# Optimization experiments

Measured on AMD Instinct MI355X. Metric: run time of the kernel, lower is better.

## Reference

```python
import jax, jax.numpy as jnp
import numpy as np

NUM_HEADS = 16
D_MODEL = 1024
D_K = 64
D_V = 64
NEG_INF = -1e9


def setup_inputs() -> dict:
    key = jax.random.key(0)
    ks = jax.random.split(key, 7)
    B, S = 2, 2048
    Q = jax.random.normal(ks[0], (B, S, D_MODEL), dtype=jnp.float32)
    K = jax.random.normal(ks[1], (B, S, D_MODEL), dtype=jnp.float32)
    V = jax.random.normal(ks[2], (B, S, D_MODEL), dtype=jnp.float32)
    s = 1.0 / np.sqrt(D_MODEL)
    W_q = jax.random.normal(ks[3], (D_MODEL, D_K * NUM_HEADS), dtype=jnp.float32) * s
    W_k = jax.random.normal(ks[4], (D_MODEL, D_K), dtype=jnp.float32) * s
    W_v = jax.random.normal(ks[5], (D_MODEL, D_V), dtype=jnp.float32) * s
    W_o = jax.random.normal(ks[6], (D_V * NUM_HEADS, D_MODEL), dtype=jnp.float32) * (1.0 / np.sqrt(D_V * NUM_HEADS))
    return {"Q": Q, "K": K, "V": V, "W_q": W_q, "W_k": W_k, "W_v": W_v, "W_o": W_o}


def reference(Q, K, V, W_q, W_k, W_v, W_o):
    B, Sq, _ = Q.shape
    Sk = K.shape[1]
    # projections: Q -> per-head, K/V -> single shared head (MQA)
    q = (Q @ W_q).reshape(B, Sq, NUM_HEADS, D_K).transpose(0, 2, 1, 3)  # [B,H,Sq,Dk]
    k = K @ W_k  # [B,Sk,Dk]
    v = V @ W_v  # [B,Sk,Dv]
    scores = jnp.einsum('bhqd,bkd->bhqk', q, k) / jnp.sqrt(jnp.float32(D_K))
    causal = jnp.tril(jnp.ones((Sq, Sk), dtype=bool))  # [Sq,Sk]
    scores = jnp.where(causal[None, None], scores, NEG_INF)
    attn = jax.nn.softmax(scores, axis=-1)  # [B,H,Sq,Sk]
    out = jnp.einsum('bhqk,bkd->bhqd', attn, v)  # [B,H,Sq,Dv]
    out = out.transpose(0, 2, 1, 3).reshape(B, Sq, NUM_HEADS * D_V)
    return out @ W_o
```

## Files before the change

kernel.cpp:

```cpp
#include <hip/hip_runtime.h>
#include <hip/hip_bf16.h>
#include <cstdint>

typedef __bf16 bf16_t;
typedef __bf16 bf16x8 __attribute__((ext_vector_type(8)));
typedef __bf16 bf16x4 __attribute__((ext_vector_type(4)));
typedef float  floatx4 __attribute__((ext_vector_type(4)));

__device__ __forceinline__ bf16_t f2bf(float x) { return (bf16_t)x; }

__device__ __forceinline__ void gll16(const void* g, void* l) {
  __builtin_amdgcn_global_load_lds((const __attribute__((address_space(1))) void*)g,
                                   (__attribute__((address_space(3))) void*)l, 16, 0, 0);
}

#define S_LEN 2048
#define NHEAD 16
#define NTILE 32

__global__ __launch_bounds__(256) void cvt_bf16(const float* __restrict__ in,
                                                bf16_t* __restrict__ out, int n) {
  int idx = (blockIdx.x * 256 + threadIdx.x) * 4;
  int stride = gridDim.x * 256 * 4;
  for (; idx < n; idx += stride) {
    float4 v = *(const float4*)(in + idx);
    bf16x4 o;
    o[0] = f2bf(v.x); o[1] = f2bf(v.y); o[2] = f2bf(v.z); o[3] = f2bf(v.w);
    *(bf16x4*)(out + idx) = o;
  }
}

__global__ __launch_bounds__(256) void transpose_w2(const float* __restrict__ W0,
                                                    const float* __restrict__ W1,
                                                    bf16_t* __restrict__ O0,
                                                    bf16_t* __restrict__ O1,
                                                    int K, int N) {
  const float* W = blockIdx.z ? W1 : W0;
  bf16_t* Wt = blockIdx.z ? O1 : O0;
  __shared__ float tile[32][33];
  int n0 = blockIdx.x * 32, k0 = blockIdx.y * 32;
  int tx = threadIdx.x & 31, ty = threadIdx.x >> 5;
#pragma unroll
  for (int r = 0; r < 4; ++r)
    tile[ty + 8 * r][tx] = W[(size_t)(k0 + ty + 8 * r) * N + n0 + tx];
  __syncthreads();
#pragma unroll
  for (int r = 0; r < 4; ++r)
    Wt[(size_t)(n0 + ty + 8 * r) * K + k0 + tx] = f2bf(tile[tx][ty + 8 * r]);
}

template <int OUTMODE>
__global__ __launch_bounds__(256, 2) void gemm_async(const bf16_t* __restrict__ A,
                                                     const bf16_t* __restrict__ Bt,
                                                     void* __restrict__ Cout,
                                                     int M, int N, int K) {
  constexpr int BK = 32;
  __shared__ __align__(16) bf16_t As[64 * BK];
  __shared__ __align__(16) bf16_t Bs[128 * BK];
  const int tid = threadIdx.x;
  const int wave = tid >> 6, lane = tid & 63;
  const int quad = lane >> 4, lm = lane & 15;
  const int wr = wave >> 1, wc = wave & 1;
  const int m0 = blockIdx.x * 64, n0 = blockIdx.y * 128;

  floatx4 acc[2][4];
#pragma unroll
  for (int i = 0; i < 2; ++i)
#pragma unroll
    for (int j = 0; j < 4; ++j) acc[i][j] = (floatx4){0.f, 0.f, 0.f, 0.f};

  for (int k0 = 0; k0 < K; k0 += BK) {
    {
      int row = tid >> 2, c8 = tid & 3;
      gll16(A + (size_t)(m0 + row) * K + k0 + c8 * 8, As + wave * 512);
    }
#pragma unroll
    for (int rd = 0; rd < 2; ++rd) {
      int idx = rd * 256 + tid, row = idx >> 2, c8 = idx & 3;
      gll16(Bt + (size_t)(n0 + row) * K + k0 + c8 * 8, Bs + rd * 2048 + wave * 512);
    }
    __syncthreads();
    bf16x8 af[2], bfr[4];
#pragma unroll
    for (int i = 0; i < 2; ++i)
      af[i] = *(const bf16x8*)&As[(wr * 32 + i * 16 + lm) * BK + quad * 8];
#pragma unroll
    for (int j = 0; j < 4; ++j)
      bfr[j] = *(const bf16x8*)&Bs[(wc * 64 + j * 16 + lm) * BK + quad * 8];
#pragma unroll
    for (int i = 0; i < 2; ++i)
#pragma unroll
      for (int j = 0; j < 4; ++j)
        acc[i][j] = __builtin_amdgcn_mfma_f32_16x16x32_bf16(af[i], bfr[j],
                                                            acc[i][j], 0, 0, 0);
    __syncthreads();
  }
#pragma unroll
  for (int i = 0; i < 2; ++i) {
#pragma unroll
    for (int j = 0; j < 4; ++j) {
      int row0 = m0 + wr * 32 + i * 16 + quad * 4;
      int col = n0 + wc * 64 + j * 16 + lm;
#pragma unroll
      for (int r = 0; r < 4; ++r) {
        if constexpr (OUTMODE == 3)
          ((bf16_t*)Cout)[(size_t)(row0 + r) * N + col] = f2bf(acc[i][j][r] * 0.125f);
        else
          ((float*)Cout)[(size_t)(row0 + r) * N + col] = acc[i][j][r];
      }
    }
  }
}

__global__ __launch_bounds__(256) void gemm_kv(const float* __restrict__ Kin,
                                               const float* __restrict__ Vin,
                                               const bf16_t* __restrict__ Wkt,
                                               const bf16_t* __restrict__ Wvt,
                                               bf16_t* __restrict__ kp,
                                               bf16_t* __restrict__ vpt,
                                               int M, int K) {
  constexpr int BK = 32, LDK = 40, N = 64;
  const int isV = blockIdx.z;
  const float* A32 = isV ? Vin : Kin;
  const bf16_t* Bt = isV ? Wvt : Wkt;
  __shared__ __align__(16) bf16_t As[64 * LDK];
  __shared__ __align__(16) bf16_t Bs[64 * LDK];
  const int tid = threadIdx.x;
  const int wave = tid >> 6, lane = tid & 63;
  const int quad = lane >> 4, lm = lane & 15;
  const int wr = wave >> 1, wc = wave & 1;
  const int m0 = blockIdx.x * 64;

  floatx4 acc[2][2];
#pragma unroll
  for (int i = 0; i < 2; ++i)
#pragma unroll
    for (int j = 0; j < 2; ++j) acc[i][j] = (floatx4){0.f, 0.f, 0.f, 0.f};

  for (int k0 = 0; k0 < K; k0 += BK) {
    {
      int row = tid >> 2, c8 = tid & 3;
      const float* src = A32 + (size_t)(m0 + row) * K + k0 + c8 * 8;
      float4 f0 = *(const float4*)src;
      float4 f1 = *(const float4*)(src + 4);
      bf16x8 o;
      o[0] = f2bf(f0.x); o[1] = f2bf(f0.y); o[2] = f2bf(f0.z); o[3] = f2bf(f0.w);
      o[4] = f2bf(f1.x); o[5] = f2bf(f1.y); o[6] = f2bf(f1.z); o[7] = f2bf(f1.w);
      *(bf16x8*)&As[row * LDK + c8 * 8] = o;
    }
    {
      int row = tid >> 2, c8 = tid & 3;
      *(bf16x8*)&Bs[row * LDK + c8 * 8] =
          *(const bf16x8*)(Bt + (size_t)row * K + k0 + c8 * 8);
    }
    __syncthreads();
    bf16x8 af[2], bfr[2];
#pragma unroll
    for (int i = 0; i < 2; ++i)
      af[i] = *(const bf16x8*)&As[(wr * 32 + i * 16 + lm) * LDK + quad * 8];
#pragma unroll
    for (int j = 0; j < 2; ++j)
      bfr[j] = *(const bf16x8*)&Bs[(wc * 32 + j * 16 + lm) * LDK + quad * 8];
#pragma unroll
    for (int i = 0; i < 2; ++i)
#pragma unroll
      for (int j = 0; j < 2; ++j)
        acc[i][j] = __builtin_amdgcn_mfma_f32_16x16x32_bf16(af[i], bfr[j],
                                                            acc[i][j], 0, 0, 0);
    __syncthreads();
  }
#pragma unroll
  for (int i = 0; i < 2; ++i) {
#pragma unroll
    for (int j = 0; j < 2; ++j) {
      int row0 = m0 + wr * 32 + i * 16 + quad * 4;
      int col = wc * 32 + j * 16 + lm;
      if (isV) {
        bf16x4 o;
#pragma unroll
        for (int r = 0; r < 4; ++r) o[r] = f2bf(acc[i][j][r]);
        *(bf16x4*)&vpt[(size_t)col * M + row0] = o;
      } else {
#pragma unroll
        for (int r = 0; r < 4; ++r)
          kp[(size_t)(row0 + r) * N + col] = f2bf(acc[i][j][r]);
      }
    }
  }
}

__global__ __launch_bounds__(256, 2) void flash_mqa(const bf16_t* __restrict__ q,
                                                    const bf16_t* __restrict__ kk,
                                                    const bf16_t* __restrict__ vt,
                                                    bf16_t* __restrict__ O,
                                                    int BStot) {
  const int ta = blockIdx.x;
  const int tb = NTILE - 1 - ta;
  const int h = blockIdx.y, b = blockIdx.z;
  const int tid = threadIdx.x;
  const int wave = tid >> 6, lane = tid & 63;
  const int quad = lane >> 4, lm = lane & 15;

  __shared__ __align__(16) bf16_t k_lds[2][64 * 72];
  __shared__ __align__(16) bf16_t vt_lds[2][64 * 72];
  __shared__ __align__(16) bf16_t p_lds[4][16 * 72];

  const size_t bS = (size_t)b * S_LEN;
  const int qa = ta * 64, qb = tb * 64;

  bf16x8 qaf[2][2];
  {
    const bf16_t* qpA = q + (bS + qa + wave * 16 + lm) * 1024 + h * 64;
    const bf16_t* qpB = q + (bS + qb + wave * 16 + lm) * 1024 + h * 64;
    qaf[0][0] = *(const bf16x8*)(qpA + quad * 8);
    qaf[0][1] = *(const bf16x8*)(qpA + 32 + quad * 8);
    qaf[1][0] = *(const bf16x8*)(qpB + quad * 8);
    qaf[1][1] = *(const bf16x8*)(qpB + 32 + quad * 8);
  }

  bf16x8 onesf;
#pragma unroll
  for (int j = 0; j < 8; ++j) onesf[j] = f2bf(1.0f);

  floatx4 acc[2][4];
  floatx4 ps[2];
#pragma unroll
  for (int c = 0; c < 2; ++c) {
    ps[c] = (floatx4){0.f, 0.f, 0.f, 0.f};
#pragma unroll
    for (int t = 0; t < 4; ++t) acc[c][t] = (floatx4){0.f, 0.f, 0.f, 0.f};
  }

  const int srow = tid >> 3, sc8 = tid & 7;
  bf16x8 kst[2], vst[2];
  auto load_kv = [&](int kt) {
    const int k0 = kt * 64;
#pragma unroll
    for (int it = 0; it < 2; ++it) {
      int r = it * 32 + srow;
      kst[it] = *(const bf16x8*)(kk + (bS + k0 + r) * 64 + sc8 * 8);
      vst[it] = *(const bf16x8*)(vt + (size_t)r * BStot + bS + k0 + sc8 * 8);
    }
  };
  auto write_kv = [&](int buf) {
#pragma unroll
    for (int it = 0; it < 2; ++it) {
      int r = it * 32 + srow;
      *(bf16x8*)&k_lds[buf][r * 72 + sc8 * 8] = kst[it];
      *(bf16x8*)&vt_lds[buf][r * 72 + sc8 * 8] = vst[it];
    }
  };

  load_kv(0);
  write_kv(0);
  __syncthreads();

  for (int kt = 0; kt <= tb; ++kt) {
    const int cur = kt & 1;
    const int k0 = kt * 64;
    if (kt < tb) load_kv(kt + 1);

#pragma unroll
    for (int c = 0; c < 2; ++c) {
      const int myt = c ? tb : ta;
      if (kt > myt) continue;
      const int qrow0 = myt * 64 + wave * 16 + quad * 4;

      floatx4 s[4];
#pragma unroll
      for (int t = 0; t < 4; ++t) {
        const bf16_t* kb = &k_lds[cur][(t * 16 + lm) * 72 + quad * 8];
        bf16x8 b0 = *(const bf16x8*)kb;
        bf16x8 b1 = *(const bf16x8*)(kb + 32);
        floatx4 cc = (floatx4){0.f, 0.f, 0.f, 0.f};
        cc = __builtin_amdgcn_mfma_f32_16x16x32_bf16(qaf[c][0], b0, cc, 0, 0, 0);
        cc = __builtin_amdgcn_mfma_f32_16x16x32_bf16(qaf[c][1], b1, cc, 0, 0, 0);
        s[t] = cc;
      }
      if (kt == myt) {
#pragma unroll
        for (int t = 0; t < 4; ++t) {
          int kj = k0 + t * 16 + lm;
#pragma unroll
          for (int r = 0; r < 4; ++r)
            s[t][r] = (kj <= qrow0 + r) ? __expf(s[t][r]) : 0.f;
        }
      } else {
#pragma unroll
        for (int t = 0; t < 4; ++t)
#pragma unroll
          for (int r = 0; r < 4; ++r) s[t][r] = __expf(s[t][r]);
      }
#pragma unroll
      for (int t = 0; t < 4; ++t)
#pragma unroll
        for (int r = 0; r < 4; ++r)
          p_lds[wave][(quad * 4 + r) * 72 + t * 16 + lm] = f2bf(s[t][r]);

      bf16x8 a0 = *(const bf16x8*)&p_lds[wave][lm * 72 + quad * 8];
      bf16x8 a1 = *(const bf16x8*)&p_lds[wave][lm * 72 + 32 + quad * 8];
      ps[c] = __builtin_amdgcn_mfma_f32_16x16x32_bf16(a0, onesf, ps[c], 0, 0, 0);
      ps[c] = __builtin_amdgcn_mfma_f32_16x16x32_bf16(a1, onesf, ps[c], 0, 0, 0);
#pragma unroll
      for (int t = 0; t < 4; ++t) {
        bf16x8 v0 = *(const bf16x8*)&vt_lds[cur][(t * 16 + lm) * 72 + quad * 8];
        bf16x8 v1 = *(const bf16x8*)&vt_lds[cur][(t * 16 + lm) * 72 + 32 + quad * 8];
        acc[c][t] = __builtin_amdgcn_mfma_f32_16x16x32_bf16(a0, v0, acc[c][t], 0, 0, 0);
        acc[c][t] = __builtin_amdgcn_mfma_f32_16x16x32_bf16(a1, v1, acc[c][t], 0, 0, 0);
      }
    }
    if (kt < tb) write_kv(1 - cur);
    __syncthreads();
  }

#pragma unroll
  for (int c = 0; c < 2; ++c) {
    const int q0 = (c ? qb : qa) + wave * 16 + quad * 4;
    float rl[4];
#pragma unroll
    for (int r = 0; r < 4; ++r) rl[r] = 1.0f / ps[c][r];
#pragma unroll
    for (int t = 0; t < 4; ++t)
#pragma unroll
      for (int r = 0; r < 4; ++r)
        O[(bS + q0 + r) * 1024 + h * 64 + t * 16 + lm] = f2bf(acc[c][t][r] * rl[r]);
  }
}

extern "C" void kernel_launch(void* const* d_in, const int* in_sizes, int n_in,
                              void* d_out, int out_size, void* d_ws, size_t ws_size,
                              hipStream_t stream) {
  const float* Q  = (const float*)d_in[0];
  const float* K  = (const float*)d_in[1];
  const float* V  = (const float*)d_in[2];
  const float* Wq = (const float*)d_in[3];
  const float* Wk = (const float*)d_in[4];
  const float* Wv = (const float*)d_in[5];
  const float* Wo = (const float*)d_in[6];

  const int BS = in_sizes[0] / 1024;
  const int B  = BS / S_LEN;

  bf16_t* ws  = (bf16_t*)d_ws;
  bf16_t* Qbf = ws;
  bf16_t* qp  = Qbf + (size_t)BS * 1024;
  bf16_t* Ob  = qp  + (size_t)BS * 1024;
  bf16_t* Wqt = Ob  + (size_t)BS * 1024;
  bf16_t* Wot = Wqt + (size_t)1024 * 1024;
  bf16_t* Wkt = Wot + (size_t)1024 * 1024;
  bf16_t* Wvt = Wkt + (size_t)64 * 1024;
  bf16_t* kp  = Wvt + (size_t)64 * 1024;
  bf16_t* vpt = kp  + (size_t)BS * 64;

  const int n = BS * 1024;
  cvt_bf16<<<1024, 256, 0, stream>>>(Q, Qbf, n);
  transpose_w2<<<dim3(32, 32, 2), 256, 0, stream>>>(Wq, Wo, Wqt, Wot, 1024, 1024);
  transpose_w2<<<dim3(2, 32, 2),  256, 0, stream>>>(Wk, Wv, Wkt, Wvt, 1024, 64);

  gemm_kv<<<dim3(BS / 64, 1, 2), 256, 0, stream>>>(K, V, Wkt, Wvt, kp, vpt, BS, 1024);

  gemm_async<3><<<dim3(BS / 64, 8), 256, 0, stream>>>(Qbf, Wqt, qp, BS, 1024, 1024);

  flash_mqa<<<dim3(NTILE / 2, NHEAD, B), 256, 0, stream>>>(qp, kp, vpt, Ob, BS);

  gemm_async<0><<<dim3(BS / 64, 8), 256, 0, stream>>>(Ob, Wot, (float*)d_out, BS, 1024, 1024);
}
```

Measured before the change: 218.9 us.

## Fuse Q fp32 conversion into GEMM, swizzle LDS, one-tile flash blocks

```diff
diff --git a/kernel.cpp b/kernel.cpp
--- a/kernel.cpp
+++ b/kernel.cpp
@@ -17,18 +17,6 @@
 #define S_LEN 2048
 #define NHEAD 16
 #define NTILE 32
-
-__global__ __launch_bounds__(256) void cvt_bf16(const float* __restrict__ in,
-                                                bf16_t* __restrict__ out, int n) {
-  int idx = (blockIdx.x * 256 + threadIdx.x) * 4;
-  int stride = gridDim.x * 256 * 4;
-  for (; idx < n; idx += stride) {
-    float4 v = *(const float4*)(in + idx);
-    bf16x4 o;
-    o[0] = f2bf(v.x); o[1] = f2bf(v.y); o[2] = f2bf(v.z); o[3] = f2bf(v.w);
-    *(bf16x4*)(out + idx) = o;
-  }
-}
 
 __global__ __launch_bounds__(256) void transpose_w2(const float* __restrict__ W0,
                                                     const float* __restrict__ W1,
@@ -49,12 +37,12 @@
     Wt[(size_t)(n0 + ty + 8 * r) * K + k0 + tx] = f2bf(tile[tx][ty + 8 * r]);
 }
 
-template <int OUTMODE>
-__global__ __launch_bounds__(256, 2) void gemm_async(const bf16_t* __restrict__ A,
+template <int OUTMODE, bool A_FP32>
+__global__ __launch_bounds__(256, 2) void gemm_async(const void* __restrict__ Ain,
                                                      const bf16_t* __restrict__ Bt,
                                                      void* __restrict__ Cout,
                                                      int M, int N, int K) {
-  constexpr int BK = 32;
+  constexpr int BK = 64;
   __shared__ __align__(16) bf16_t As[64 * BK];
   __shared__ __align__(16) bf16_t Bs[128 * BK];
   const int tid = threadIdx.x;
@@ -70,29 +58,55 @@
     for (int j = 0; j < 4; ++j) acc[i][j] = (floatx4){0.f, 0.f, 0.f, 0.f};
 
   for (int k0 = 0; k0 < K; k0 += BK) {
-    {
-      int row = tid >> 2, c8 = tid & 3;
-      gll16(A + (size_t)(m0 + row) * K + k0 + c8 * 8, As + wave * 512);
-    }
-#pragma unroll
-    for (int rd = 0; rd < 2; ++rd) {
-      int idx = rd * 256 + tid, row = idx >> 2, c8 = idx & 3;
-      gll16(Bt + (size_t)(n0 + row) * K + k0 + c8 * 8, Bs + rd * 2048 + wave * 512);
-    }
-    __syncthreads();
-    bf16x8 af[2], bfr[4];
-#pragma unroll
-    for (int i = 0; i < 2; ++i)
-      af[i] = *(const bf16x8*)&As[(wr * 32 + i * 16 + lm) * BK + quad * 8];
-#pragma unroll
-    for (int j = 0; j < 4; ++j)
-      bfr[j] = *(const bf16x8*)&Bs[(wc * 64 + j * 16 + lm) * BK + quad * 8];
-#pragma unroll
-    for (int i = 0; i < 2; ++i)
-#pragma unroll
-      for (int j = 0; j < 4; ++j)
-        acc[i][j] = __builtin_amdgcn_mfma_f32_16x16x32_bf16(af[i], bfr[j],
-                                                            acc[i][j], 0, 0, 0);
+    if constexpr (A_FP32) {
+#pragma unroll
+      for (int rd = 0; rd < 2; ++rd) {
+        int idx = rd * 256 + tid, row = idx >> 3, ch = (idx & 7) ^ (row & 7);
+        const float* src = (const float*)Ain + (size_t)(m0 + row) * K + k0 + ch * 8;
+        float4 f0 = *(const float4*)src;
+        float4 f1 = *(const float4*)(src + 4);
+        bf16x8 o;
+        o[0] = f2bf(f0.x); o[1] = f2bf(f0.y); o[2] = f2bf(f0.z); o[3] = f2bf(f0.w);
+        o[4] = f2bf(f1.x); o[5] = f2bf(f1.y); o[6] = f2bf(f1.z); o[7] = f2bf(f1.w);
+        *(bf16x8*)&As[idx * 8] = o;
+      }
+    } else {
+#pragma unroll
+      for (int rd = 0; rd < 2; ++rd) {
+        int idx = rd * 256 + tid, row = idx >> 3, ch = (idx & 7) ^ (row & 7);
+        gll16((const bf16_t*)Ain + (size_t)(m0 + row) * K + k0 + ch * 8,
+              As + (rd * 256 + wave * 64) * 8);
+      }
+    }
+#pragma unroll
+    for (int rd = 0; rd < 4; ++rd) {
+      int idx = rd * 256 + tid, row = idx >> 3, ch = (idx & 7) ^ (row & 7);
+      gll16(Bt + (size_t)(n0 + row) * K + k0 + ch * 8,
+            Bs + (rd * 256 + wave * 64) * 8);
+    }
+    __syncthreads();
+    const int sw = lm & 7;
+    bf16x8 af[2][2], bfr[4][2];
+#pragma unroll
+    for (int i = 0; i < 2; ++i) {
+      const bf16_t* base = &As[(wr * 32 + i * 16 + lm) * BK];
+      af[i][0] = *(const bf16x8*)(base + ((quad ^ sw) * 8));
+      af[i][1] = *(const bf16x8*)(base + (((4 + quad) ^ sw) * 8));
+    }
+#pragma unroll
+    for (int j = 0; j < 4; ++j) {
+      const bf16_t* base = &Bs[(wc * 64 + j * 16 + lm) * BK];
+      bfr[j][0] = *(const bf16x8*)(base + ((quad ^ sw) * 8));
+      bfr[j][1] = *(const bf16x8*)(base + (((4 + quad) ^ sw) * 8));
+    }
+#pragma unroll
+    for (int ks = 0; ks < 2; ++ks)
+#pragma unroll
+      for (int i = 0; i < 2; ++i)
+#pragma unroll
+        for (int j = 0; j < 4; ++j)
+          acc[i][j] = __builtin_amdgcn_mfma_f32_16x16x32_bf16(af[i][ks], bfr[j][ks],
+                                                              acc[i][j], 0, 0, 0);
     __syncthreads();
   }
 #pragma unroll
@@ -189,49 +203,41 @@
   }
 }
 
-__global__ __launch_bounds__(256, 2) void flash_mqa(const bf16_t* __restrict__ q,
+__global__ __launch_bounds__(256, 4) void flash_mqa(const bf16_t* __restrict__ q,
                                                     const bf16_t* __restrict__ kk,
                                                     const bf16_t* __restrict__ vt,
                                                     bf16_t* __restrict__ O,
                                                     int BStot) {
-  const int ta = blockIdx.x;
-  const int tb = NTILE - 1 - ta;
+  const int qt = NTILE - 1 - blockIdx.x;
   const int h = blockIdx.y, b = blockIdx.z;
   const int tid = threadIdx.x;
   const int wave = tid >> 6, lane = tid & 63;
   const int quad = lane >> 4, lm = lane & 15;
 
-  __shared__ __align__(16) bf16_t k_lds[2][64 * 72];
-  __shared__ __align__(16) bf16_t vt_lds[2][64 * 72];
-  __shared__ __align__(16) bf16_t p_lds[4][16 * 72];
+  __shared__ __align__(16) bf16_t k_lds[2][64 * 64];
+  __shared__ __align__(16) bf16_t vt_lds[2][64 * 64];
+  __shared__ __align__(16) bf16_t p_lds[4][16 * 64];
 
   const size_t bS = (size_t)b * S_LEN;
-  const int qa = ta * 64, qb = tb * 64;
-
-  bf16x8 qaf[2][2];
+  const int qb = qt * 64;
+
+  bf16x8 qf[2];
   {
-    const bf16_t* qpA = q + (bS + qa + wave * 16 + lm) * 1024 + h * 64;
-    const bf16_t* qpB = q + (bS + qb + wave * 16 + lm) * 1024 + h * 64;
-    qaf[0][0] = *(const bf16x8*)(qpA + quad * 8);
-    qaf[0][1] = *(const bf16x8*)(qpA + 32 + quad * 8);
-    qaf[1][0] = *(const bf16x8*)(qpB + quad * 8);
-    qaf[1][1] = *(const bf16x8*)(qpB + 32 + quad * 8);
-  }
-
+    const bf16_t* qp = q + (bS + qb + wave * 16 + lm) * 1024 + h * 64;
+    qf[0] = *(const bf16x8*)(qp + quad * 8);
+    qf[1] = *(const bf16x8*)(qp + 32 + quad * 8);
+  }
   bf16x8 onesf;
 #pragma unroll
   for (int j = 0; j < 8; ++j) onesf[j] = f2bf(1.0f);
 
-  floatx4 acc[2][4];
-  floatx4 ps[2];
-#pragma unroll
-  for (int c = 0; c < 2; ++c) {
-    ps[c] = (floatx4){0.f, 0.f, 0.f, 0.f};
-#pragma unroll
-    for (int t = 0; t < 4; ++t) acc[c][t] = (floatx4){0.f, 0.f, 0.f, 0.f};
-  }
+  floatx4 acc[4];
+  floatx4 ps = (floatx4){0.f, 0.f, 0.f, 0.f};
+#pragma unroll
+  for (int t = 0; t < 4; ++t) acc[t] = (floatx4){0.f, 0.f, 0.f, 0.f};
 
   const int srow = tid >> 3, sc8 = tid & 7;
+  const int swst = (sc8 ^ (srow & 7)) * 8;
   bf16x8 kst[2], vst[2];
   auto load_kv = [&](int kt) {
     const int k0 = kt * 64;
@@ -246,8 +252,8 @@
 #pragma unroll
     for (int it = 0; it < 2; ++it) {
       int r = it * 32 + srow;
-      *(bf16x8*)&k_lds[buf][r * 72 + sc8 * 8] = kst[it];
-      *(bf16x8*)&vt_lds[buf][r * 72 + sc8 * 8] = vst[it];
+      *(bf16x8*)&k_lds[buf][r * 64 + swst] = kst[it];
+      *(bf16x8*)&vt_lds[buf][r * 64 + swst] = vst[it];
     }
   };
 
@@ -255,76 +261,70 @@
   write_kv(0);
   __syncthreads();
 
-  for (int kt = 0; kt <= tb; ++kt) {
+  const int sw = lm & 7;
+  const int qloc = wave * 16 + lm;
+
+  for (int kt = 0; kt <= qt; ++kt) {
     const int cur = kt & 1;
-    const int k0 = kt * 64;
-    if (kt < tb) load_kv(kt + 1);
-
-#pragma unroll
-    for (int c = 0; c < 2; ++c) {
-      const int myt = c ? tb : ta;
-      if (kt > myt) continue;
-      const int qrow0 = myt * 64 + wave * 16 + quad * 4;
-
-      floatx4 s[4];
-#pragma unroll
-      for (int t = 0; t < 4; ++t) {
-        const bf16_t* kb = &k_lds[cur][(t * 16 + lm) * 72 + quad * 8];
-        bf16x8 b0 = *(const bf16x8*)kb;
-        bf16x8 b1 = *(const bf16x8*)(kb + 32);
-        floatx4 cc = (floatx4){0.f, 0.f, 0.f, 0.f};
-        cc = __builtin_amdgcn_mfma_f32_16x16x32_bf16(qaf[c][0], b0, cc, 0, 0, 0);
-        cc = __builtin_amdgcn_mfma_f32_16x16x32_bf16(qaf[c][1], b1, cc, 0, 0, 0);
-        s[t] = cc;
-      }
-      if (kt == myt) {
-#pragma unroll
-        for (int t = 0; t < 4; ++t) {
-          int kj = k0 + t * 16 + lm;
-#pragma unroll
-          for (int r = 0; r < 4; ++r)
-            s[t][r] = (kj <= qrow0 + r) ? __expf(s[t][r]) : 0.f;
+    if (kt < qt) load_kv(kt + 1);
+
+    floatx4 s[4];
+#pragma unroll
+    for (int t = 0; t < 4; ++t) {
+      const bf16_t* kb = &k_lds[cur][(t * 16 + lm) * 64];
+      bf16x8 a0 = *(const bf16x8*)(kb + ((quad ^ sw) * 8));
+      bf16x8 a1 = *(const bf16x8*)(kb + (((4 + quad) ^ sw) * 8));
+      floatx4 cc = (floatx4){0.f, 0.f, 0.f, 0.f};
+      cc = __builtin_amdgcn_mfma_f32_16x16x32_bf16(a0, qf[0], cc, 0, 0, 0);
+      cc = __builtin_amdgcn_mfma_f32_16x16x32_bf16(a1, qf[1], cc, 0, 0, 0);
+      s[t] = cc;
+    }
+    if (kt == qt) {
+#pragma unroll
+      for (int t = 0; t < 4; ++t)
+#pragma unroll
+        for (int r = 0; r < 4; ++r) {
+          int kj = t * 16 + quad * 4 + r;
+          s[t][r] = (kj <= qloc) ? __expf(s[t][r]) : 0.f;
         }
-      } else {
-#pragma unroll
-        for (int t = 0; t < 4; ++t)
-#pragma unroll
-          for (int r = 0; r < 4; ++r) s[t][r] = __expf(s[t][r]);
-      }
+    } else {
 #pragma unroll
       for (int t = 0; t < 4; ++t)
 #pragma unroll
-        for (int r = 0; r < 4; ++r)
-          p_lds[wave][(quad * 4 + r) * 72 + t * 16 + lm] = f2bf(s[t][r]);
-
-      bf16x8 a0 = *(const bf16x8*)&p_lds[wave][lm * 72 + quad * 8];
-      bf16x8 a1 = *(const bf16x8*)&p_lds[wave][lm * 72 + 32 + quad * 8];
-      ps[c] = __builtin_amdgcn_mfma_f32_16x16x32_bf16(a0, onesf, ps[c], 0, 0, 0);
-      ps[c] = __builtin_amdgcn_mfma_f32_16x16x32_bf16(a1, onesf, ps[c], 0, 0, 0);
-#pragma unroll
-      for (int t = 0; t < 4; ++t) {
-        bf16x8 v0 = *(const bf16x8*)&vt_lds[cur][(t * 16 + lm) * 72 + quad * 8];
-        bf16x8 v1 = *(const bf16x8*)&vt_lds[cur][(t * 16 + lm) * 72 + 32 + quad * 8];
-        acc[c][t] = __builtin_amdgcn_mfma_f32_16x16x32_bf16(a0, v0, acc[c][t], 0, 0, 0);
-        acc[c][t] = __builtin_amdgcn_mfma_f32_16x16x32_bf16(a1, v1, acc[c][t], 0, 0, 0);
-      }
-    }
-    if (kt < tb) write_kv(1 - cur);
-    __syncthreads();
-  }
-
-#pragma unroll
-  for (int c = 0; c < 2; ++c) {
-    const int q0 = (c ? qb : qa) + wave * 16 + quad * 4;
-    float rl[4];
-#pragma unroll
-    for (int r = 0; r < 4; ++r) rl[r] = 1.0f / ps[c][r];
-#pragma unroll
-    for (int t = 0; t < 4; ++t)
-#pragma unroll
-      for (int r = 0; r < 4; ++r)
-        O[(bS + q0 + r) * 1024 + h * 64 + t * 16 + lm] = f2bf(acc[c][t][r] * rl[r]);
-  }
+        for (int r = 0; r < 4; ++r) s[t][r] = __expf(s[t][r]);
+    }
+#pragma unroll
+    for (int t = 0; t < 4; ++t) {
+      bf16x4 pk;
+#pragma unroll
+      for (int r = 0; r < 4; ++r) pk[r] = f2bf(s[t][r]);
+      *(bf16x4*)&p_lds[wave][lm * 64 + (((2 * t + (quad >> 1)) ^ sw) * 8) + (quad & 1) * 4] = pk;
+    }
+    bf16x8 p0 = *(const bf16x8*)&p_lds[wave][lm * 64 + ((quad ^ sw) * 8)];
+    bf16x8 p1 = *(const bf16x8*)&p_lds[wave][lm * 64 + (((4 + quad) ^ sw) * 8)];
+    ps = __builtin_amdgcn_mfma_f32_16x16x32_bf16(p0, onesf, ps, 0, 0, 0);
+    ps = __builtin_amdgcn_mfma_f32_16x16x32_bf16(p1, onesf, ps, 0, 0, 0);
+#pragma unroll
+    for (int t = 0; t < 4; ++t) {
+      const bf16_t* vb = &vt_lds[cur][(t * 16 + lm) * 64];
+      bf16x8 v0 = *(const bf16x8*)(vb + ((quad ^ sw) * 8));
+      bf16x8 v1 = *(const bf16x8*)(vb + (((4 + quad) ^ sw) * 8));
+      acc[t] = __builtin_amdgcn_mfma_f32_16x16x32_bf16(p0, v0, acc[t], 0, 0, 0);
+      acc[t] = __builtin_amdgcn_mfma_f32_16x16x32_bf16(p1, v1, acc[t], 0, 0, 0);
+    }
+    if (kt < qt) write_kv(1 - cur);
+    __syncthreads();
+  }
+
+  float rl[4];
+#pragma unroll
+  for (int r = 0; r < 4; ++r) rl[r] = 1.0f / ps[r];
+  const int q0 = qb + wave * 16 + quad * 4;
+#pragma unroll
+  for (int t = 0; t < 4; ++t)
+#pragma unroll
+    for (int r = 0; r < 4; ++r)
+      O[(bS + q0 + r) * 1024 + h * 64 + t * 16 + lm] = f2bf(acc[t][r] * rl[r]);
 }
 
 extern "C" void kernel_launch(void* const* d_in, const int* in_sizes, int n_in,
@@ -342,8 +342,7 @@
   const int B  = BS / S_LEN;
 
   bf16_t* ws  = (bf16_t*)d_ws;
-  bf16_t* Qbf = ws;
-  bf16_t* qp  = Qbf + (size_t)BS * 1024;
+  bf16_t* qp  = ws;
   bf16_t* Ob  = qp  + (size_t)BS * 1024;
   bf16_t* Wqt = Ob  + (size_t)BS * 1024;
   bf16_t* Wot = Wqt + (size_t)1024 * 1024;
@@ -352,16 +351,14 @@
   bf16_t* kp  = Wvt + (size_t)64 * 1024;
   bf16_t* vpt = kp  + (size_t)BS * 64;
 
-  const int n = BS * 1024;
-  cvt_bf16<<<1024, 256, 0, stream>>>(Q, Qbf, n);
   transpose_w2<<<dim3(32, 32, 2), 256, 0, stream>>>(Wq, Wo, Wqt, Wot, 1024, 1024);
   transpose_w2<<<dim3(2, 32, 2),  256, 0, stream>>>(Wk, Wv, Wkt, Wvt, 1024, 64);
 
   gemm_kv<<<dim3(BS / 64, 1, 2), 256, 0, stream>>>(K, V, Wkt, Wvt, kp, vpt, BS, 1024);
 
-  gemm_async<3><<<dim3(BS / 64, 8), 256, 0, stream>>>(Qbf, Wqt, qp, BS, 1024, 1024);
-
-  flash_mqa<<<dim3(NTILE / 2, NHEAD, B), 256, 0, stream>>>(qp, kp, vpt, Ob, BS);
-
-  gemm_async<0><<<dim3(BS / 64, 8), 256, 0, stream>>>(Ob, Wot, (float*)d_out, BS, 1024, 1024);
-}
+  gemm_async<3, true><<<dim3(BS / 64, 8), 256, 0, stream>>>(Q, Wqt, qp, BS, 1024, 1024);
+
+  flash_mqa<<<dim3(NTILE, NHEAD, B), 256, 0, stream>>>(qp, kp, vpt, Ob, BS);
+
+  gemm_async<0, false><<<dim3(BS / 64, 8), 256, 0, stream>>>(Ob, Wot, (float*)d_out, BS, 1024, 1024);
+}
```

Result: no change. 216.5 us (-1.1%).
